# Performance work log

Hardware: AMD Instinct MI355X
Metric: run time of the kernel (lower is better)

Reference implementation:

```python
import jax, jax.numpy as jnp
import numpy as np

K = 16  # neighbors per node (knn_graph, loop=False)


def setup_inputs() -> dict:
    key = jax.random.key(0)
    ks = jax.random.split(key, 4)
    B, N = 32, 2048
    coords = jax.random.normal(ks[0], (B, N, 3), jnp.float32)

    def lin(k, i, o):  # glorot-ish init
        return jax.random.normal(k, (i, o), jnp.float32) / np.sqrt(i).astype(np.float32)

    return {
        "coords": coords,
        "W1": lin(ks[1], 3, 64),   "b1": jnp.zeros((64,), jnp.float32),
        "W2": lin(ks[2], 64, 128), "b2": jnp.zeros((128,), jnp.float32),
        "Wf": lin(ks[3], 128, 128), "bf": jnp.zeros((128,), jnp.float32),
    }


def _knn_idx(c, k):
    # c: [N,3] -> [N,k] indices of k nearest neighbors (self excluded, loop=False)
    n = c.shape[0]
    d2 = jnp.sum((c[:, None, :] - c[None, :, :]) ** 2, axis=-1)  # [N,N]
    d2 = jnp.where(jnp.eye(n, dtype=bool), jnp.inf, d2)
    _, idx = jax.lax.top_k(-d2, k)  # smallest distances
    return idx


def _gcn(x, nbr_self, W, b):
    # PyG GCNConv with add_self_loops: every node has in-degree exactly k+1
    # (k knn edges + self-loop), so the symmetric gcn_norm
    # 1/sqrt(deg_i*deg_j) reduces to the constant 1/(k+1).
    h = x @ W                                   # [N,out]
    agg = h[nbr_self].sum(axis=1) / nbr_self.shape[1]
    return agg + b


def reference(coords, W1, b1, W2, b2, Wf, bf):
    n = coords.shape[1]

    def per_sample(c):
        nbr = _knn_idx(c, K)                                     # [N,K]
        nbr_self = jnp.concatenate([nbr, jnp.arange(n)[:, None]], axis=1)  # [N,K+1]
        x = jax.nn.relu(_gcn(c, nbr_self, W1, b1))
        x = jax.nn.relu(_gcn(x, nbr_self, W2, b2))
        return x @ Wf + bf                                       # [N,128]

    return jax.vmap(per_sample)(coords)  # [B,N,128]
```

## Files before the change

### kernel.cpp

```cpp
#include <hip/hip_runtime.h>
#include <hip/hip_bf16.h>

typedef unsigned int u32;
typedef __attribute__((ext_vector_type(8))) short bf16x8;
typedef __attribute__((ext_vector_type(4))) float f32x4;

#define N_NODES 2048
#define INF __builtin_inff()

__device__ __forceinline__ float bflo(u32 u){ return __uint_as_float(u << 16); }
__device__ __forceinline__ float bfhi(u32 u){ return __uint_as_float(u & 0xFFFF0000u); }
__device__ __forceinline__ u32 packbf(float a, float b){
  u32 ua = __float_as_uint(a), ub = __float_as_uint(b);
  u32 ra = (ua + 0x7FFFu + ((ua >> 16) & 1u)) >> 16;
  u32 rb = (ub + 0x7FFFu + ((ub >> 16) & 1u)) >> 16;
  return ra | (rb << 16);
}

__device__ __forceinline__ float dist2(float cx, float cy, float cz,
                                       float jx, float jy, float jz) {
  float dx = cx - jx, dy = cy - jy, dz = cz - jz;
  return fmaf(dz, dz, fmaf(dy, dy, dx * dx));
}

__device__ __forceinline__ float mkk(float d, int j) {
  return __uint_as_float((__float_as_uint(d) & 0xFFFFF800u) | (u32)j);
}

__device__ __forceinline__ void ins8(float (&ad)[8], float v) {
#pragma unroll
  for (int t = 7; t >= 1; --t)
    ad[t] = __builtin_amdgcn_fmed3f(v, ad[t-1], ad[t]);
  ad[0] = fminf(ad[0], v);
}
__device__ __forceinline__ void ins16(float (&ad)[16], float v) {
#pragma unroll
  for (int t = 15; t >= 1; --t)
    ad[t] = __builtin_amdgcn_fmed3f(v, ad[t-1], ad[t]);
  ad[0] = fminf(ad[0], v);
}

__device__ __forceinline__ void merge8s(float (&ad)[16], int tid) {
#define CED(I, J) { float lo_ = fminf(ad[I], ad[J]); ad[J] = fmaxf(ad[I], ad[J]); ad[I] = lo_; }
#define CLEAN16 \
  CED(0,8) CED(1,9) CED(2,10) CED(3,11) CED(4,12) CED(5,13) CED(6,14) CED(7,15) \
  CED(0,4) CED(1,5) CED(2,6)  CED(3,7)  CED(8,12) CED(9,13) CED(10,14) CED(11,15) \
  CED(0,2) CED(1,3) CED(4,6)  CED(5,7)  CED(8,10) CED(9,11) CED(12,14) CED(13,15) \
  CED(0,1) CED(2,3) CED(4,5)  CED(6,7)  CED(8,9)  CED(10,11) CED(12,13) CED(14,15)
  float bd[16];
#pragma unroll
  for (int q = 0; q < 16; ++q) bd[q] = __shfl(ad[q], tid ^ 1);
#pragma unroll
  for (int q = 0; q < 16; ++q) ad[q] = fminf(ad[q], bd[15 - q]);
  CLEAN16
#pragma unroll
  for (int q = 0; q < 16; ++q) bd[q] = __shfl(ad[q], tid ^ 2);
#pragma unroll
  for (int q = 0; q < 16; ++q) ad[q] = fminf(ad[q], bd[15 - q]);
  CLEAN16
#pragma unroll
  for (int q = 0; q < 16; ++q) bd[q] = __shfl(ad[q], tid ^ 4);
#pragma unroll
  for (int q = 0; q < 16; ++q) ad[q] = fminf(ad[q], bd[15 - q]);
  CLEAN16
#undef CLEAN16
#undef CED
}

__device__ __forceinline__ bool node_try8(
    const float (&ad)[8], int tid, int sub, int& j0, int& j1)
{
  const float myMax = ad[7];
  float md[16];
#pragma unroll
  for (int q = 0; q < 8; ++q) md[q] = ad[q];
#pragma unroll
  for (int q = 8; q < 16; ++q) md[q] = __uint_as_float(0x7F000000u);
  merge8s(md, tid);
  const float md15 = md[15];
  float mnext = INF;
#pragma unroll
  for (int q = 7; q >= 0; --q) mnext = (ad[q] > md15) ? ad[q] : mnext;
  float c17 = fminf(mnext, __shfl(mnext, tid ^ 1));
  c17 = fminf(c17, __shfl(c17, tid ^ 2));
  c17 = fminf(c17, __shfl(c17, tid ^ 4));
  float mnext2 = INF;
#pragma unroll
  for (int q = 7; q >= 0; --q) mnext2 = (ad[q] > c17) ? ad[q] : mnext2;
  float c18 = fminf(mnext2, __shfl(mnext2, tid ^ 1));
  c18 = fminf(c18, __shfl(c18, tid ^ 2));
  c18 = fminf(c18, __shfl(c18, tid ^ 4));
  const u32 t17 = __float_as_uint(c17) & 0xFFFFF800u;
  const u32 t18 = __float_as_uint(c18) & 0xFFFFF800u;
  md[0] = c17;
  j0 = (int)(__float_as_uint(md[(sub<<1)+0]) & 0x7FFu);
  j1 = (int)(__float_as_uint(md[(sub<<1)+1]) & 0x7FFu);
  return (myMax >= c18) && (t18 >= t17 + 0x800u);
}

__device__ __forceinline__ void node_fb8(
    int node, int tid, int sub, int slot,
    float cx, float cy, float cz, const float* cs,
    u32 (*nbuf)[16], u32* ncnt, int& j0, int& j1)
{
  float a3[16];
#pragma unroll
  for (int q = 0; q < 16; ++q) a3[q] = INF;
#pragma unroll 1
  for (int it = 0; it < 64; ++it) {
    const int v4 = (it << 3) + sub;
    const float4* p = (const float4*)(cs + v4 * 12);
    float4 p0 = p[0], p1 = p[1], p2 = p[2];
    const int base = v4 << 2;
    float d0 = (base + 0 == node) ? INF : dist2(cx,cy,cz, p0.x,p0.y,p0.z);
    float d1 = (base + 1 == node) ? INF : dist2(cx,cy,cz, p0.w,p1.x,p1.y);
    float d2 = (base + 2 == node) ? INF : dist2(cx,cy,cz, p1.z,p1.w,p2.x);
    float d3 = (base + 3 == node) ? INF : dist2(cx,cy,cz, p2.y,p2.z,p2.w);
    ins16(a3, d0); ins16(a3, d1); ins16(a3, d2); ins16(a3, d3);
  }
  merge8s(a3, tid);
  const float tau = a3[15];
  if (sub == 0) ncnt[slot] = 0;
  asm volatile("s_waitcnt lgkmcnt(0)" ::: "memory");
#pragma unroll 1
  for (int it = 0; it < 64; ++it) {
    const int v4 = (it << 3) + sub;
    const float4* p = (const float4*)(cs + v4 * 12);
    float4 p0 = p[0], p1 = p[1], p2 = p[2];
    const int base = v4 << 2;
    float d0 = dist2(cx,cy,cz, p0.x,p0.y,p0.z);
    float d1 = dist2(cx,cy,cz, p0.w,p1.x,p1.y);
    float d2 = dist2(cx,cy,cz, p1.z,p1.w,p2.x);
    float d3 = dist2(cx,cy,cz, p2.y,p2.z,p2.w);
    if (d0 <= tau && base + 0 != node) { u32 p_ = atomicAdd(&ncnt[slot], 1u); if (p_ < 16u) nbuf[slot][p_] = (u32)(base + 0); }
    if (d1 <= tau && base + 1 != node) { u32 p_ = atomicAdd(&ncnt[slot], 1u); if (p_ < 16u) nbuf[slot][p_] = (u32)(base + 1); }
    if (d2 <= tau && base + 2 != node) { u32 p_ = atomicAdd(&ncnt[slot], 1u); if (p_ < 16u) nbuf[slot][p_] = (u32)(base + 2); }
    if (d3 <= tau && base + 3 != node) { u32 p_ = atomicAdd(&ncnt[slot], 1u); if (p_ < 16u) nbuf[slot][p_] = (u32)(base + 3); }
  }
  asm volatile("s_waitcnt lgkmcnt(0)" ::: "memory");
  j0 = (int)nbuf[slot][(sub << 1) + 0];
  j1 = (int)nbuf[slot][(sub << 1) + 1];
}

__global__ __launch_bounds__(512) void k1_knn_l1(
    const float* __restrict__ coords, const float* __restrict__ W1,
    const float* __restrict__ b1, int* __restrict__ nbr, u32* __restrict__ x1)
{
  __shared__ float ldsc[N_NODES * 3];
  __shared__ u32   nbuf[64][16];
  __shared__ u32   ncnt[64];
  __shared__ float w1s[192];
  __shared__ float b1s[64];
  const int tid   = threadIdx.x;
  const int s     = blockIdx.x >> 5;
  const int chunk = blockIdx.x & 31;
  const float* cg = coords + (size_t)s * (N_NODES * 3);
  {
    const float4* src = (const float4*)cg;
    float4* dst = (float4*)ldsc;
#pragma unroll
    for (int q = 0; q < 3; ++q) dst[tid + (q << 9)] = src[tid + (q << 9)];
  }
  if (tid < 192) w1s[tid] = W1[tid];
  if (tid < 64)  b1s[tid] = b1[tid];
  __syncthreads();

  const int ln   = tid >> 3;
  const int sub  = tid & 7;
  const int node = (chunk << 6) + ln;
  const float cx = ldsc[3*node], cy = ldsc[3*node+1], cz = ldsc[3*node+2];

  float ad[8];
#pragma unroll
  for (int q = 0; q < 8; ++q) ad[q] = INF;

#define LOAD6(P0,P1,P2,P3,P4,P5, ITV) {                                   \
    const int v4a_ = ((ITV) << 4) + sub;                                  \
    const float4* pa_ = (const float4*)(ldsc + v4a_ * 12);                \
    const float4* pb_ = (const float4*)(ldsc + (v4a_ + 8) * 12);          \
    P0 = pa_[0]; P1 = pa_[1]; P2 = pa_[2];                                \
    P3 = pb_[0]; P4 = pb_[1]; P5 = pb_[2]; }

#define BODY(P0,P1,P2,P3,P4,P5, ITV) {                                    \
    const int ba_ = (((ITV) << 4) + sub) << 2, bb_ = ba_ + 32;            \
    ins8(ad, mkk(dist2(cx,cy,cz, P0.x,P0.y,P0.z),   ba_+0));              \
    ins8(ad, mkk(dist2(cx,cy,cz, P0.w,P1.x,P1.y),   ba_+1));              \
    ins8(ad, mkk(dist2(cx,cy,cz, P1.z,P1.w,P2.x),   ba_+2));              \
    ins8(ad, mkk(dist2(cx,cy,cz, P2.y,P2.z,P2.w),   ba_+3));              \
    ins8(ad, mkk(dist2(cx,cy,cz, P3.x,P3.y,P3.z),   bb_+0));              \
    ins8(ad, mkk(dist2(cx,cy,cz, P3.w,P4.x,P4.y),   bb_+1));              \
    ins8(ad, mkk(dist2(cx,cy,cz, P4.z,P4.w,P5.x),   bb_+2));              \
    ins8(ad, mkk(dist2(cx,cy,cz, P5.y,P5.z,P5.w),   bb_+3)); }

  {
    float4 A0, A1, A2, A3, A4, A5, B0, B1, B2, B3, B4, B5;
    LOAD6(A0,A1,A2,A3,A4,A5, 0)
#pragma unroll 1
    for (int it = 0; it < 32; it += 2) {
      LOAD6(B0,B1,B2,B3,B4,B5, it + 1)
      BODY (A0,A1,A2,A3,A4,A5, it)
      LOAD6(A0,A1,A2,A3,A4,A5, (it + 2) & 31)
      BODY (B0,B1,B2,B3,B4,B5, it + 1)
    }
  }
#undef LOAD6
#undef BODY

  int j0, j1;
  const bool ok = node_try8(ad, tid, sub, j0, j1);
  if (!__all((int)ok)) {
    node_fb8(node, tid, sub, ln, cx, cy, cz, ldsc, nbuf, ncnt, j0, j1);
  }

  const size_t gnode = ((size_t)s << 11) + node;
  *(int2*)(nbr + gnode * 16 + (sub << 1)) = make_int2(j0, j1);

  float sx, sy, sz;
  if (sub == 0) { sx = cx; sy = cy; sz = cz; } else { sx = 0.f; sy = 0.f; sz = 0.f; }
  sx += ldsc[3*j0]   + ldsc[3*j1];
  sy += ldsc[3*j0+1] + ldsc[3*j1+1];
  sz += ldsc[3*j0+2] + ldsc[3*j1+2];
  sx += __shfl_xor(sx, 1); sx += __shfl_xor(sx, 2); sx += __shfl_xor(sx, 4);
  sy += __shfl_xor(sy, 1); sy += __shfl_xor(sy, 2); sy += __shfl_xor(sy, 4);
  sz += __shfl_xor(sz, 1); sz += __shfl_xor(sz, 2); sz += __shfl_xor(sz, 4);
  const float inv = 1.0f / 17.0f;
  float mx = sx * inv, my = sy * inv, mz = sz * inv;

  u32 pk[4];
#pragma unroll
  for (int oo = 0; oo < 8; oo += 2) {
    const int o = (sub << 3) + oo;
    float v0 = fmaf(mz, w1s[128+o],   fmaf(my, w1s[64+o],   fmaf(mx, w1s[o],   b1s[o])));
    float v1 = fmaf(mz, w1s[128+o+1], fmaf(my, w1s[64+o+1], fmaf(mx, w1s[o+1], b1s[o+1])));
    pk[oo >> 1] = packbf(fmaxf(v0, 0.0f), fmaxf(v1, 0.0f));
  }
  *(uint4*)(x1 + gnode * 32 + (sub << 2)) = make_uint4(pk[0], pk[1], pk[2], pk[3]);
}

__global__ __launch_bounds__(256) void k2_gcn2(
    const u32* __restrict__ x1, const int* __restrict__ nbr,
    const float* __restrict__ W2, const float* __restrict__ b2,
    u32* __restrict__ x2)
{
  __shared__ uint4 AldsV[1024];
  __shared__ uint4 BhiV[1024];
  __shared__ uint4 BloV[1024];
  char* Alds = (char*)AldsV; char* Bhi = (char*)BhiV; char* Blo = (char*)BloV;
  const int tid   = threadIdx.x;
  const int node0 = blockIdx.x << 7;

#pragma unroll
  for (int i = 0; i < 32; ++i) {
    int e = tid + (i << 8);
    int k = e >> 7, n = e & 127;
    float w = W2[e];
    u32 hb = packbf(w, 0.0f) & 0xFFFFu;
    float whi = __uint_as_float(hb << 16);
    u32 lb = packbf(w - whi, 0.0f) & 0xFFFFu;
    int byte = n * 128 + ((2 * k) ^ ((n & 7) << 4));
    *(unsigned short*)(Bhi + byte) = (unsigned short)hb;
    *(unsigned short*)(Blo + byte) = (unsigned short)lb;
  }

  {
    const int r = tid >> 1, half = tid & 1;
    const size_t gnode = (size_t)node0 + r;
    const u32* selfp = x1 + gnode * 32 + half * 16;
    const u32* x1s   = x1 + ((gnode >> 11) << 11) * 32;
    const int* nb    = nbr + gnode * 16;
    float a[32];
#pragma unroll
    for (int q = 0; q < 4; ++q) {
      uint4 v = *(const uint4*)(selfp + (q << 2));
      a[8*q+0] = bflo(v.x); a[8*q+1] = bfhi(v.x);
      a[8*q+2] = bflo(v.y); a[8*q+3] = bfhi(v.y);
      a[8*q+4] = bflo(v.z); a[8*q+5] = bfhi(v.z);
      a[8*q+6] = bflo(v.w); a[8*q+7] = bfhi(v.w);
    }
#pragma unroll
    for (int t = 0; t < 16; ++t) {
      const u32* rp = x1s + (size_t)nb[t] * 32 + half * 16;
#pragma unroll
      for (int q = 0; q < 4; ++q) {
        uint4 v = *(const uint4*)(rp + (q << 2));
        a[8*q+0] += bflo(v.x); a[8*q+1] += bfhi(v.x);
        a[8*q+2] += bflo(v.y); a[8*q+3] += bfhi(v.y);
        a[8*q+4] += bflo(v.z); a[8*q+5] += bfhi(v.z);
        a[8*q+6] += bflo(v.w); a[8*q+7] += bfhi(v.w);
      }
    }
    const float inv = 1.0f / 17.0f;
    u32 pk[16];
#pragma unroll
    for (int j = 0; j < 16; ++j)
      pk[j] = packbf(a[2*j] * inv, a[2*j+1] * inv);
#pragma unroll
    for (int q = 0; q < 4; ++q) {
      int byte = r * 128 + ((((half << 6) + (q << 4))) ^ ((r & 7) << 4));
      *(uint4*)(Alds + byte) = make_uint4(pk[4*q], pk[4*q+1], pk[4*q+2], pk[4*q+3]);
    }
  }
  __syncthreads();

  const int lane = tid & 63, wv = tid >> 6;
  const int cl = lane & 15, kg = lane >> 4;

  f32x4 acc[2][8];
#pragma unroll
  for (int rt = 0; rt < 2; ++rt)
#pragma unroll
    for (int ct = 0; ct < 8; ++ct) {
      float bv = b2[(ct << 4) + cl];
      acc[rt][ct] = (f32x4){bv, bv, bv, bv};
    }

#pragma unroll
  for (int ks = 0; ks < 2; ++ks) {
    const int kb = (ks << 6) + (kg << 4);
    bf16x8 af[2];
#pragma unroll
    for (int rt = 0; rt < 2; ++rt) {
      int row = (wv << 5) + (rt << 4) + cl;
      af[rt] = *(const bf16x8*)(Alds + row * 128 + (kb ^ ((row & 7) << 4)));
    }
#pragma unroll
    for (int ct = 0; ct < 8; ++ct) {
      int n = (ct << 4) + cl;
      int byte = n * 128 + (kb ^ ((n & 7) << 4));
      bf16x8 bh = *(const bf16x8*)(Bhi + byte);
      bf16x8 bl = *(const bf16x8*)(Blo + byte);
#pragma unroll
      for (int rt = 0; rt < 2; ++rt) {
        acc[rt][ct] = __builtin_amdgcn_mfma_f32_16x16x32_bf16(af[rt], bh, acc[rt][ct], 0, 0, 0);
        acc[rt][ct] = __builtin_amdgcn_mfma_f32_16x16x32_bf16(af[rt], bl, acc[rt][ct], 0, 0, 0);
      }
    }
  }

  unsigned short* x2h = (unsigned short*)x2;
#pragma unroll
  for (int rt = 0; rt < 2; ++rt)
#pragma unroll
    for (int ct = 0; ct < 8; ++ct) {
      int colg = (ct << 4) + cl;
      int nr0  = node0 + (wv << 5) + (rt << 4) + (kg << 2);
#pragma unroll
      for (int r = 0; r < 4; ++r) {
        float v = fmaxf(acc[rt][ct][r], 0.0f);
        x2h[(size_t)(nr0 + r) * 128 + colg] = (unsigned short)(packbf(v, 0.0f) & 0xFFFFu);
      }
    }
}

__global__ __launch_bounds__(256) void k3_final(
    const u32* __restrict__ x2, const float* __restrict__ Wf,
    const float* __restrict__ bfv, float* __restrict__ out)
{
  __shared__ uint4 AldsV[2048];
  __shared__ uint4 BhiV[1024];
  __shared__ uint4 BloV[1024];
  char* Alds = (char*)AldsV; char* Bhi = (char*)BhiV; char* Blo = (char*)BloV;
  const int tid   = threadIdx.x;
  const int node0 = (blockIdx.x >> 1) << 7;
  const int ch0   = (blockIdx.x & 1) << 6;

#pragma unroll
  for (int i = 0; i < 32; ++i) {
    int e = tid + (i << 8);
    int k = e >> 6, n = e & 63;
    float w = Wf[k * 128 + ch0 + n];
    u32 hb = packbf(w, 0.0f) & 0xFFFFu;
    float whi = __uint_as_float(hb << 16);
    u32 lb = packbf(w - whi, 0.0f) & 0xFFFFu;
    int byte = n * 256 + ((2 * k) ^ ((n & 15) << 4));
    *(unsigned short*)(Bhi + byte) = (unsigned short)hb;
    *(unsigned short*)(Blo + byte) = (unsigned short)lb;
  }

  {
    const int r = tid >> 1, half = tid & 1;
    const u32* src = x2 + (size_t)(node0 + r) * 64 + half * 32;
#pragma unroll
    for (int q = 0; q < 8; ++q) {
      uint4 v = *(const uint4*)(src + (q << 2));
      int byte = r * 256 + ((((half << 7) + (q << 4))) ^ ((r & 15) << 4));
      *(uint4*)(Alds + byte) = v;
    }
  }
  __syncthreads();

  const int lane = tid & 63, wv = tid >> 6;
  const int cl = lane & 15, kg = lane >> 4;

  f32x4 acc[2][4];
#pragma unroll
  for (int rt = 0; rt < 2; ++rt)
#pragma unroll
    for (int ct = 0; ct < 4; ++ct) {
      float bv = bfv[ch0 + (ct << 4) + cl];
      acc[rt][ct] = (f32x4){bv, bv, bv, bv};
    }

#pragma unroll
  for (int ks = 0; ks < 4; ++ks) {
    const int kb = (ks << 6) + (kg << 4);
    bf16x8 af[2];
#pragma unroll
    for (int rt = 0; rt < 2; ++rt) {
      int row = (wv << 5) + (rt << 4) + cl;
      af[rt] = *(const bf16x8*)(Alds + row * 256 + (kb ^ ((row & 15) << 4)));
    }
#pragma unroll
    for (int ct = 0; ct < 4; ++ct) {
      int n = (ct << 4) + cl;
      int byte = n * 256 + (kb ^ ((n & 15) << 4));
      bf16x8 bh = *(const bf16x8*)(Bhi + byte);
      bf16x8 bl = *(const bf16x8*)(Blo + byte);
#pragma unroll
      for (int rt = 0; rt < 2; ++rt) {
        acc[rt][ct] = __builtin_amdgcn_mfma_f32_16x16x32_bf16(af[rt], bh, acc[rt][ct], 0, 0, 0);
        acc[rt][ct] = __builtin_amdgcn_mfma_f32_16x16x32_bf16(af[rt], bl, acc[rt][ct], 0, 0, 0);
      }
    }
  }

#pragma unroll
  for (int rt = 0; rt < 2; ++rt)
#pragma unroll
    for (int ct = 0; ct < 4; ++ct) {
      int col = ch0 + (ct << 4) + cl;
      int nr0 = node0 + (wv << 5) + (rt << 4) + (kg << 2);
#pragma unroll
      for (int r = 0; r < 4; ++r)
        out[(size_t)(nr0 + r) * 128 + col] = acc[rt][ct][r];
    }
}

extern "C" void kernel_launch(void* const* d_in, const int* in_sizes, int n_in,
                              void* d_out, int out_size, void* d_ws, size_t ws_size,
                              hipStream_t stream) {
  const float* coords = (const float*)d_in[0];
  const float* W1 = (const float*)d_in[1];
  const float* b1 = (const float*)d_in[2];
  const float* W2 = (const float*)d_in[3];
  const float* b2 = (const float*)d_in[4];
  const float* Wf = (const float*)d_in[5];
  const float* bf = (const float*)d_in[6];
  float* out = (float*)d_out;

  char* ws = (char*)d_ws;
  int* nbr = (int*)ws;
  u32* x1  = (u32*)(ws + (size_t)4  * 1024 * 1024);
  u32* x2  = (u32*)(ws + (size_t)12 * 1024 * 1024);

  k1_knn_l1<<<1024, 512, 0, stream>>>(coords, W1, b1, nbr, x1);
  k2_gcn2  <<< 512, 256, 0, stream>>>(x1, nbr, W2, b2, x2);
  k3_final <<<1024, 256, 0, stream>>>(x2, Wf, bf, out);
}
```

Baseline: 164.3 us.

## Store KNN coordinates as swizzled SoA float4 tiles in LDS

```diff
diff --git a/kernel.cpp b/kernel.cpp
--- a/kernel.cpp
+++ b/kernel.cpp
@@ -39,6 +39,8 @@
     ad[t] = __builtin_amdgcn_fmed3f(v, ad[t-1], ad[t]);
   ad[0] = fminf(ad[0], v);
 }
+
+__device__ __forceinline__ int swzq(int q){ return q ^ ((q >> 3) & 7); }
 
 __device__ __forceinline__ void merge8s(float (&ad)[16], int tid) {
 #define CED(I, J) { float lo_ = fminf(ad[I], ad[J]); ad[J] = fmaxf(ad[I], ad[J]); ad[I] = lo_; }
@@ -100,7 +102,8 @@
 
 __device__ __forceinline__ void node_fb8(
     int node, int tid, int sub, int slot,
-    float cx, float cy, float cz, const float* cs,
+    float cx, float cy, float cz,
+    const float4* xsw, const float4* ysw, const float4* zsw,
     u32 (*nbuf)[16], u32* ncnt, int& j0, int& j1)
 {
   float a3[16];
@@ -108,14 +111,14 @@
   for (int q = 0; q < 16; ++q) a3[q] = INF;
 #pragma unroll 1
   for (int it = 0; it < 64; ++it) {
-    const int v4 = (it << 3) + sub;
-    const float4* p = (const float4*)(cs + v4 * 12);
-    float4 p0 = p[0], p1 = p[1], p2 = p[2];
-    const int base = v4 << 2;
-    float d0 = (base + 0 == node) ? INF : dist2(cx,cy,cz, p0.x,p0.y,p0.z);
-    float d1 = (base + 1 == node) ? INF : dist2(cx,cy,cz, p0.w,p1.x,p1.y);
-    float d2 = (base + 2 == node) ? INF : dist2(cx,cy,cz, p1.z,p1.w,p2.x);
-    float d3 = (base + 3 == node) ? INF : dist2(cx,cy,cz, p2.y,p2.z,p2.w);
+    const int q = (it << 3) + sub;
+    const int qs = swzq(q);
+    float4 X = xsw[qs], Y = ysw[qs], Z = zsw[qs];
+    const int base = q << 2;
+    float d0 = (base + 0 == node) ? INF : dist2(cx,cy,cz, X.x,Y.x,Z.x);
+    float d1 = (base + 1 == node) ? INF : dist2(cx,cy,cz, X.y,Y.y,Z.y);
+    float d2 = (base + 2 == node) ? INF : dist2(cx,cy,cz, X.z,Y.z,Z.z);
+    float d3 = (base + 3 == node) ? INF : dist2(cx,cy,cz, X.w,Y.w,Z.w);
     ins16(a3, d0); ins16(a3, d1); ins16(a3, d2); ins16(a3, d3);
   }
   merge8s(a3, tid);
@@ -124,14 +127,14 @@
   asm volatile("s_waitcnt lgkmcnt(0)" ::: "memory");
 #pragma unroll 1
   for (int it = 0; it < 64; ++it) {
-    const int v4 = (it << 3) + sub;
-    const float4* p = (const float4*)(cs + v4 * 12);
-    float4 p0 = p[0], p1 = p[1], p2 = p[2];
-    const int base = v4 << 2;
-    float d0 = dist2(cx,cy,cz, p0.x,p0.y,p0.z);
-    float d1 = dist2(cx,cy,cz, p0.w,p1.x,p1.y);
-    float d2 = dist2(cx,cy,cz, p1.z,p1.w,p2.x);
-    float d3 = dist2(cx,cy,cz, p2.y,p2.z,p2.w);
+    const int q = (it << 3) + sub;
+    const int qs = swzq(q);
+    float4 X = xsw[qs], Y = ysw[qs], Z = zsw[qs];
+    const int base = q << 2;
+    float d0 = dist2(cx,cy,cz, X.x,Y.x,Z.x);
+    float d1 = dist2(cx,cy,cz, X.y,Y.y,Z.y);
+    float d2 = dist2(cx,cy,cz, X.z,Y.z,Z.z);
+    float d3 = dist2(cx,cy,cz, X.w,Y.w,Z.w);
     if (d0 <= tau && base + 0 != node) { u32 p_ = atomicAdd(&ncnt[slot], 1u); if (p_ < 16u) nbuf[slot][p_] = (u32)(base + 0); }
     if (d1 <= tau && base + 1 != node) { u32 p_ = atomicAdd(&ncnt[slot], 1u); if (p_ < 16u) nbuf[slot][p_] = (u32)(base + 1); }
     if (d2 <= tau && base + 2 != node) { u32 p_ = atomicAdd(&ncnt[slot], 1u); if (p_ < 16u) nbuf[slot][p_] = (u32)(base + 2); }
@@ -146,70 +149,75 @@
     const float* __restrict__ coords, const float* __restrict__ W1,
     const float* __restrict__ b1, int* __restrict__ nbr, u32* __restrict__ x1)
 {
-  __shared__ float ldsc[N_NODES * 3];
-  __shared__ u32   nbuf[64][16];
-  __shared__ u32   ncnt[64];
-  __shared__ float w1s[192];
-  __shared__ float b1s[64];
+  __shared__ float4 xsw[512], ysw[512], zsw[512];
+  __shared__ u32    nbuf[64][16];
+  __shared__ u32    ncnt[64];
+  __shared__ float  w1s[192];
+  __shared__ float  b1s[64];
   const int tid   = threadIdx.x;
   const int s     = blockIdx.x >> 5;
   const int chunk = blockIdx.x & 31;
   const float* cg = coords + (size_t)s * (N_NODES * 3);
   {
-    const float4* src = (const float4*)cg;
-    float4* dst = (float4*)ldsc;
-#pragma unroll
-    for (int q = 0; q < 3; ++q) dst[tid + (q << 9)] = src[tid + (q << 9)];
+    const float4* src = (const float4*)(cg + 12 * tid);
+    float4 v0 = src[0], v1 = src[1], v2 = src[2];
+    const int qs = swzq(tid);
+    xsw[qs] = make_float4(v0.x, v0.w, v1.z, v2.y);
+    ysw[qs] = make_float4(v0.y, v1.x, v1.w, v2.z);
+    zsw[qs] = make_float4(v0.z, v1.y, v2.x, v2.w);
   }
   if (tid < 192) w1s[tid] = W1[tid];
   if (tid < 64)  b1s[tid] = b1[tid];
   __syncthreads();
 
   const int ln   = tid >> 3;
+  const int g    = ln & 7;
   const int sub  = tid & 7;
   const int node = (chunk << 6) + ln;
-  const float cx = ldsc[3*node], cy = ldsc[3*node+1], cz = ldsc[3*node+2];
+  float cx, cy, cz;
+  {
+    const int sq = node >> 2, se = node & 3, sqs = swzq(sq);
+    cx = ((const float*)&xsw[sqs])[se];
+    cy = ((const float*)&ysw[sqs])[se];
+    cz = ((const float*)&zsw[sqs])[se];
+  }
+
+  const int qbase = (sub << 6) + (g << 3);
 
   float ad[8];
 #pragma unroll
   for (int q = 0; q < 8; ++q) ad[q] = INF;
 
-#define LOAD6(P0,P1,P2,P3,P4,P5, ITV) {                                   \
-    const int v4a_ = ((ITV) << 4) + sub;                                  \
-    const float4* pa_ = (const float4*)(ldsc + v4a_ * 12);                \
-    const float4* pb_ = (const float4*)(ldsc + (v4a_ + 8) * 12);          \
-    P0 = pa_[0]; P1 = pa_[1]; P2 = pa_[2];                                \
-    P3 = pb_[0]; P4 = pb_[1]; P5 = pb_[2]; }
-
-#define BODY(P0,P1,P2,P3,P4,P5, ITV) {                                    \
-    const int ba_ = (((ITV) << 4) + sub) << 2, bb_ = ba_ + 32;            \
-    ins8(ad, mkk(dist2(cx,cy,cz, P0.x,P0.y,P0.z),   ba_+0));              \
-    ins8(ad, mkk(dist2(cx,cy,cz, P0.w,P1.x,P1.y),   ba_+1));              \
-    ins8(ad, mkk(dist2(cx,cy,cz, P1.z,P1.w,P2.x),   ba_+2));              \
-    ins8(ad, mkk(dist2(cx,cy,cz, P2.y,P2.z,P2.w),   ba_+3));              \
-    ins8(ad, mkk(dist2(cx,cy,cz, P3.x,P3.y,P3.z),   bb_+0));              \
-    ins8(ad, mkk(dist2(cx,cy,cz, P3.w,P4.x,P4.y),   bb_+1));              \
-    ins8(ad, mkk(dist2(cx,cy,cz, P4.z,P4.w,P5.x),   bb_+2));              \
-    ins8(ad, mkk(dist2(cx,cy,cz, P5.y,P5.z,P5.w),   bb_+3)); }
-
-  {
-    float4 A0, A1, A2, A3, A4, A5, B0, B1, B2, B3, B4, B5;
-    LOAD6(A0,A1,A2,A3,A4,A5, 0)
+#define LOAD3(PX,PY,PZ, I) {                                              \
+    const int q_ = (qbase + (I)) & 511;                                   \
+    const int qs_ = swzq(q_);                                             \
+    PX = xsw[qs_]; PY = ysw[qs_]; PZ = zsw[qs_]; }
+
+#define BODY(PX,PY,PZ, I) {                                               \
+    const int jb_ = ((qbase + (I)) & 511) << 2;                           \
+    ins8(ad, mkk(dist2(cx,cy,cz, PX.x,PY.x,PZ.x), jb_+0));                \
+    ins8(ad, mkk(dist2(cx,cy,cz, PX.y,PY.y,PZ.y), jb_+1));                \
+    ins8(ad, mkk(dist2(cx,cy,cz, PX.z,PY.z,PZ.z), jb_+2));                \
+    ins8(ad, mkk(dist2(cx,cy,cz, PX.w,PY.w,PZ.w), jb_+3)); }
+
+  {
+    float4 AX, AY, AZ, BX, BY, BZ;
+    LOAD3(AX,AY,AZ, 0)
 #pragma unroll 1
-    for (int it = 0; it < 32; it += 2) {
-      LOAD6(B0,B1,B2,B3,B4,B5, it + 1)
-      BODY (A0,A1,A2,A3,A4,A5, it)
-      LOAD6(A0,A1,A2,A3,A4,A5, (it + 2) & 31)
-      BODY (B0,B1,B2,B3,B4,B5, it + 1)
-    }
-  }
-#undef LOAD6
+    for (int i = 0; i < 64; i += 2) {
+      LOAD3(BX,BY,BZ, i + 1)
+      BODY (AX,AY,AZ, i)
+      LOAD3(AX,AY,AZ, (i + 2) & 63)
+      BODY (BX,BY,BZ, i + 1)
+    }
+  }
+#undef LOAD3
 #undef BODY
 
   int j0, j1;
   const bool ok = node_try8(ad, tid, sub, j0, j1);
   if (!__all((int)ok)) {
-    node_fb8(node, tid, sub, ln, cx, cy, cz, ldsc, nbuf, ncnt, j0, j1);
+    node_fb8(node, tid, sub, ln, cx, cy, cz, xsw, ysw, zsw, nbuf, ncnt, j0, j1);
   }
 
   const size_t gnode = ((size_t)s << 11) + node;
@@ -217,9 +225,13 @@
 
   float sx, sy, sz;
   if (sub == 0) { sx = cx; sy = cy; sz = cz; } else { sx = 0.f; sy = 0.f; sz = 0.f; }
-  sx += ldsc[3*j0]   + ldsc[3*j1];
-  sy += ldsc[3*j0+1] + ldsc[3*j1+1];
-  sz += ldsc[3*j0+2] + ldsc[3*j1+2];
+  {
+    const int q0 = j0 >> 2, e0 = j0 & 3, qs0 = swzq(q0);
+    const int q1 = j1 >> 2, e1 = j1 & 3, qs1 = swzq(q1);
+    sx += ((const float*)&xsw[qs0])[e0] + ((const float*)&xsw[qs1])[e1];
+    sy += ((const float*)&ysw[qs0])[e0] + ((const float*)&ysw[qs1])[e1];
+    sz += ((const float*)&zsw[qs0])[e0] + ((const float*)&zsw[qs1])[e1];
+  }
   sx += __shfl_xor(sx, 1); sx += __shfl_xor(sx, 2); sx += __shfl_xor(sx, 4);
   sy += __shfl_xor(sy, 1); sy += __shfl_xor(sy, 2); sy += __shfl_xor(sy, 4);
   sz += __shfl_xor(sz, 1); sz += __shfl_xor(sz, 2); sz += __shfl_xor(sz, 4);
```

After: 169.6 us. +3.2%, slower.

## Split per-lane top-8 into four independent top-6 chains and halve k1 block size

Applied to the files above, without the earlier changes.

```diff
diff --git a/kernel.cpp b/kernel.cpp
--- a/kernel.cpp
+++ b/kernel.cpp
@@ -27,6 +27,12 @@
   return __uint_as_float((__float_as_uint(d) & 0xFFFFF800u) | (u32)j);
 }
 
+__device__ __forceinline__ void ins6(float (&ad)[6], float v) {
+#pragma unroll
+  for (int t = 5; t >= 1; --t)
+    ad[t] = __builtin_amdgcn_fmed3f(v, ad[t-1], ad[t]);
+  ad[0] = fminf(ad[0], v);
+}
 __device__ __forceinline__ void ins8(float (&ad)[8], float v) {
 #pragma unroll
   for (int t = 7; t >= 1; --t)
@@ -68,7 +74,7 @@
 }
 
 __device__ __forceinline__ bool node_try8(
-    const float (&ad)[8], int tid, int sub, int& j0, int& j1)
+    const float (&ad)[8], float mn4, int tid, int sub, int& j0, int& j1)
 {
   const float myMax = ad[7];
   float md[16];
@@ -95,7 +101,7 @@
   md[0] = c17;
   j0 = (int)(__float_as_uint(md[(sub<<1)+0]) & 0x7FFu);
   j1 = (int)(__float_as_uint(md[(sub<<1)+1]) & 0x7FFu);
-  return (myMax >= c18) && (t18 >= t17 + 0x800u);
+  return (myMax >= c18) && (mn4 >= c18) && (t18 >= t17 + 0x800u);
 }
 
 __device__ __forceinline__ void node_fb8(
@@ -142,24 +148,24 @@
   j1 = (int)nbuf[slot][(sub << 1) + 1];
 }
 
-__global__ __launch_bounds__(512) void k1_knn_l1(
+__global__ __launch_bounds__(256) void k1_knn_l1(
     const float* __restrict__ coords, const float* __restrict__ W1,
     const float* __restrict__ b1, int* __restrict__ nbr, u32* __restrict__ x1)
 {
   __shared__ float ldsc[N_NODES * 3];
-  __shared__ u32   nbuf[64][16];
-  __shared__ u32   ncnt[64];
+  __shared__ u32   nbuf[32][16];
+  __shared__ u32   ncnt[32];
   __shared__ float w1s[192];
   __shared__ float b1s[64];
   const int tid   = threadIdx.x;
-  const int s     = blockIdx.x >> 5;
-  const int chunk = blockIdx.x & 31;
+  const int s     = blockIdx.x >> 6;
+  const int chunk = blockIdx.x & 63;
   const float* cg = coords + (size_t)s * (N_NODES * 3);
   {
     const float4* src = (const float4*)cg;
     float4* dst = (float4*)ldsc;
 #pragma unroll
-    for (int q = 0; q < 3; ++q) dst[tid + (q << 9)] = src[tid + (q << 9)];
+    for (int q = 0; q < 6; ++q) dst[tid + (q << 8)] = src[tid + (q << 8)];
   }
   if (tid < 192) w1s[tid] = W1[tid];
   if (tid < 64)  b1s[tid] = b1[tid];
@@ -167,12 +173,12 @@
 
   const int ln   = tid >> 3;
   const int sub  = tid & 7;
-  const int node = (chunk << 6) + ln;
+  const int node = (chunk << 5) + ln;
   const float cx = ldsc[3*node], cy = ldsc[3*node+1], cz = ldsc[3*node+2];
 
-  float ad[8];
-#pragma unroll
-  for (int q = 0; q < 8; ++q) ad[q] = INF;
+  float c0[6], c1[6], c2[6], c3[6];
+#pragma unroll
+  for (int q = 0; q < 6; ++q) { c0[q] = INF; c1[q] = INF; c2[q] = INF; c3[q] = INF; }
 
 #define LOAD6(P0,P1,P2,P3,P4,P5, ITV) {                                   \
     const int v4a_ = ((ITV) << 4) + sub;                                  \
@@ -183,14 +189,14 @@
 
 #define BODY(P0,P1,P2,P3,P4,P5, ITV) {                                    \
     const int ba_ = (((ITV) << 4) + sub) << 2, bb_ = ba_ + 32;            \
-    ins8(ad, mkk(dist2(cx,cy,cz, P0.x,P0.y,P0.z),   ba_+0));              \
-    ins8(ad, mkk(dist2(cx,cy,cz, P0.w,P1.x,P1.y),   ba_+1));              \
-    ins8(ad, mkk(dist2(cx,cy,cz, P1.z,P1.w,P2.x),   ba_+2));              \
-    ins8(ad, mkk(dist2(cx,cy,cz, P2.y,P2.z,P2.w),   ba_+3));              \
-    ins8(ad, mkk(dist2(cx,cy,cz, P3.x,P3.y,P3.z),   bb_+0));              \
-    ins8(ad, mkk(dist2(cx,cy,cz, P3.w,P4.x,P4.y),   bb_+1));              \
-    ins8(ad, mkk(dist2(cx,cy,cz, P4.z,P4.w,P5.x),   bb_+2));              \
-    ins8(ad, mkk(dist2(cx,cy,cz, P5.y,P5.z,P5.w),   bb_+3)); }
+    ins6(c0, mkk(dist2(cx,cy,cz, P0.x,P0.y,P0.z),   ba_+0));              \
+    ins6(c1, mkk(dist2(cx,cy,cz, P0.w,P1.x,P1.y),   ba_+1));              \
+    ins6(c2, mkk(dist2(cx,cy,cz, P1.z,P1.w,P2.x),   ba_+2));              \
+    ins6(c3, mkk(dist2(cx,cy,cz, P2.y,P2.z,P2.w),   ba_+3));              \
+    ins6(c0, mkk(dist2(cx,cy,cz, P3.x,P3.y,P3.z),   bb_+0));              \
+    ins6(c1, mkk(dist2(cx,cy,cz, P3.w,P4.x,P4.y),   bb_+1));              \
+    ins6(c2, mkk(dist2(cx,cy,cz, P4.z,P4.w,P5.x),   bb_+2));              \
+    ins6(c3, mkk(dist2(cx,cy,cz, P5.y,P5.z,P5.w),   bb_+3)); }
 
   {
     float4 A0, A1, A2, A3, A4, A5, B0, B1, B2, B3, B4, B5;
@@ -206,8 +212,17 @@
 #undef LOAD6
 #undef BODY
 
+  float ad[8];
+#pragma unroll
+  for (int q = 0; q < 8; ++q) ad[q] = INF;
+#pragma unroll
+  for (int q = 0; q < 6; ++q) {
+    ins8(ad, c0[q]); ins8(ad, c1[q]); ins8(ad, c2[q]); ins8(ad, c3[q]);
+  }
+  const float mn4 = fminf(fminf(c0[5], c1[5]), fminf(c2[5], c3[5]));
+
   int j0, j1;
-  const bool ok = node_try8(ad, tid, sub, j0, j1);
+  const bool ok = node_try8(ad, mn4, tid, sub, j0, j1);
   if (!__all((int)ok)) {
     node_fb8(node, tid, sub, ln, cx, cy, cz, ldsc, nbuf, ncnt, j0, j1);
   }
@@ -453,7 +468,7 @@
   u32* x1  = (u32*)(ws + (size_t)4  * 1024 * 1024);
   u32* x2  = (u32*)(ws + (size_t)12 * 1024 * 1024);
 
-  k1_knn_l1<<<1024, 512, 0, stream>>>(coords, W1, b1, nbr, x1);
+  k1_knn_l1<<<2048, 256, 0, stream>>>(coords, W1, b1, nbr, x1);
   k2_gcn2  <<< 512, 256, 0, stream>>>(x1, nbr, W2, b2, x2);
   k3_final <<<1024, 256, 0, stream>>>(x2, Wf, bf, out);
 }
```

Measured after the change: 156.7 us (median of 3 runs). 4.6% less time.
